# Optimization experiments

Measured on AMD Instinct MI355X. Metric: run time of the kernel, lower is better.

Reference implementation:

```python
import jax, jax.numpy as jnp
import numpy as np
from jax import lax


def _shifted(X, k, alpha):
    # alpha * roll(X, -k, 0) + (1 - alpha) * roll(X, -k-1, 0), via gather
    N = X.shape[0]
    idx = (jnp.arange(N) + k) % N
    return alpha * X[idx] + (1.0 - alpha) * X[(idx + 1) % N]


def _all_distances(D_q, D_p, steps):
    # steps: [S] float32 signed step values. Returns [S] mean L2 distances.
    N = D_q.shape[0]
    rows = jnp.arange(N)

    def dist_one(step):
        s = jnp.abs(step)
        k = jnp.floor(s).astype(jnp.int32)          # int(step) of |step|
        alpha = s - k.astype(step.dtype)
        diff = lax.cond(
            step >= 0,
            lambda: _shifted(D_q, k, alpha) - D_p,   # shift query forward
            lambda: D_q - _shifted(D_p, k, alpha),   # shift positive (ref) forward
        )
        norms = jnp.sqrt(jnp.sum(diff * diff, axis=-1))  # [N]
        valid = rows < (N - k)                       # rows [:N - int_step]
        return jnp.sum(jnp.where(valid, norms, 0.0)) / (N - k).astype(norms.dtype)

    def body(carry, step):
        return carry, dist_one(step)

    _, dists = lax.scan(body, None, steps)
    return dists


def setup_inputs() -> dict:
    key = jax.random.key(0)
    k1, k2 = jax.random.split(key)
    N, D = 100000, 256
    return {
        "D_q": jax.random.normal(k1, (N, D), dtype=jnp.float32),
        "D_p": jax.random.normal(k2, (N, D), dtype=jnp.float32),
        "max_step": 60,
        "step_size": 1,
    }


def reference(D_q, D_p, max_step, step_size):
    # Same candidate step schedule as the torch loop (static, built on host).
    steps_np = np.concatenate([
        np.arange(0, max_step, step_size),
        -np.arange(1, max_step + 1, step_size),
    ]).astype(np.float32)
    steps = jnp.asarray(steps_np)                    # [2*max_step/step_size]
    dists = _all_distances(D_q, D_p, steps)
    i = jnp.argmin(dists)
    return steps[i], dists[i]
```

## Files before the change

kernel.cpp:

```cpp
#include <hip/hip_runtime.h>
#include <math.h>


typedef __attribute__((ext_vector_type(8))) __bf16 bf16x8;
typedef __attribute__((ext_vector_type(16))) float f32x16;
typedef __attribute__((ext_vector_type(8))) unsigned short us8;

#define LDSH 280
#define PR 6
#define MAXS 128
#define NREP 32

#define LGKM_FENCE()                                                          \
  do {                                                                        \
    __builtin_amdgcn_sched_barrier(0);                                        \
    asm volatile("s_waitcnt lgkmcnt(0)" ::: "memory");                        \
    __builtin_amdgcn_sched_barrier(0);                                        \
  } while (0)

__device__ __forceinline__ unsigned short f2bf(float x) {
  return __builtin_bit_cast(unsigned short, (__bf16)x);
}

__device__ __forceinline__ int xcd_swz(int bid, int nwg) {
  const int q = nwg >> 3, r = nwg & 7;
  const int x = bid & 7, i = bid >> 3;
  return (x < r ? x * (q + 1) : r * (q + 1) + (x - r) * q) + i;
}

__global__ __launch_bounds__(576, 1)
void band_kernel(const float* __restrict__ Q, const float* __restrict__ P,
                 double* __restrict__ ws,
                 const int* __restrict__ msp, const int* __restrict__ ssp,
                 int N, int TS, int nsb, int gridB) {
  __shared__ __align__(16) unsigned short Bsh[PR * 32 * LDSH];
  __shared__ __align__(16) unsigned short Qsh[2 * 32 * LDSH];
  __shared__ float NpS[PR * 32];
  __shared__ float NqS[2 * 32];
  __shared__ float sums[MAXS];
  __shared__ float red[12];
  __shared__ int packs[2];

  const int t = threadIdx.x;
  const int lane = t & 63;
  const int wid = t >> 6;
  const int ms = msp[0], ss = ssp[0];
  const int S1 = (ms + ss - 1) / ss;
  const int S = 2 * S1;

  if (blockIdx.x >= gridB) {
    const int si = blockIdx.x - gridB;
    if (si >= S) return;
    int k, qr, pr;
    if (si < S1) { k = si * ss;            qr = 0;           pr = N - (k + 1); }
    else         { k = 1 + (si - S1) * ss; qr = N - (k + 1); pr = 0; }
    float sq = 0.f;
    if (t < 256) {
      const float e = Q[(size_t)qr * 256 + t] - P[(size_t)pr * 256 + t];
      sq = e * e;
    }
    #pragma unroll
    for (int off = 32; off >= 1; off >>= 1) sq += __shfl_xor(sq, off);
    if (lane == 0) red[wid] = sq;
    __syncthreads();
    if (t == 0) {
      float tot = 0.f;
      #pragma unroll
      for (int w = 0; w < 9; ++w) tot += red[w];
      ws[(size_t)NREP * MAXS + si] = (double)sqrtf(tot);
    }
    return;
  }

  const int sb = xcd_swz(blockIdx.x, gridB);
  const int T0 = sb * nsb;
  int ns = TS - T0; if (ns > nsb) ns = nsb;
  if (ns <= 0) return;

  for (int i = t; i < MAXS; i += 576) sums[i] = 0.f;
  if (t == 0) { packs[0] = 0; packs[1] = 0; }
  __syncthreads();

  volatile int* vprod = &packs[0];
  volatile int* vcons = &packs[1];

  if (wid >= 5) {
    const int pw = wid - 5;
    const int rr = pw * 8 + (lane >> 3);
    const int li = lane & 7;

    auto issueT = [&](const float* __restrict__ base, int tau, float4* v) {
      const int gr = tau * 32 + rr;
      if (gr >= 0 && gr < N) {
        const float* src = base + (size_t)gr * 256 + li * 8;
        #pragma unroll
        for (int j = 0; j < 4; ++j) {
          v[2 * j]     = *reinterpret_cast<const float4*>(src + j * 64);
          v[2 * j + 1] = *reinterpret_cast<const float4*>(src + j * 64 + 4);
        }
      } else {
        #pragma unroll
        for (int j = 0; j < 8; ++j) v[j] = make_float4(0.f, 0.f, 0.f, 0.f);
      }
    };

    auto commitT = [&](unsigned short* dst, float* ndst, int slot, const float4* v) {
      float nrm = 0.f;
      unsigned short* row = dst + slot * 32 * LDSH + rr * LDSH + li * 8;
      #pragma unroll
      for (int j = 0; j < 4; ++j) {
        const float f0 = v[2*j].x, f1 = v[2*j].y, f2 = v[2*j].z, f3 = v[2*j].w;
        const float f4 = v[2*j+1].x, f5 = v[2*j+1].y, f6 = v[2*j+1].z, f7 = v[2*j+1].w;
        nrm = fmaf(f0, f0, nrm); nrm = fmaf(f1, f1, nrm);
        nrm = fmaf(f2, f2, nrm); nrm = fmaf(f3, f3, nrm);
        nrm = fmaf(f4, f4, nrm); nrm = fmaf(f5, f5, nrm);
        nrm = fmaf(f6, f6, nrm); nrm = fmaf(f7, f7, nrm);
        us8 h;
        h[0] = f2bf(f0); h[1] = f2bf(f1); h[2] = f2bf(f2); h[3] = f2bf(f3);
        h[4] = f2bf(f4); h[5] = f2bf(f5); h[6] = f2bf(f6); h[7] = f2bf(f7);
        *reinterpret_cast<us8*>(row + j * 64) = h;
      }
      nrm += __shfl_xor(nrm, 1);
      nrm += __shfl_xor(nrm, 2);
      nrm += __shfl_xor(nrm, 4);
      if (li == 0) ndst[slot * 32 + rr] = nrm;
    };

    float4 Ap[8], Aq[8], Bp[8], Bq[8];
    const int JT = ns + 4;

#define P_ISSUE(JJ, SET)                                                      \
    { const int pj_ = (JJ);                                                   \
      if (pj_ < JT) {                                                         \
        issueT(P, T0 + pj_ - 2, SET##p);                                      \
        if (pj_ >= 4) issueT(Q, T0 + pj_ - 4, SET##q);                        \
      } }
#define P_STEP(JJ, SET)                                                       \
    { const int j_ = (JJ);                                                    \
      const int needc = j_ - 5;                                               \
      if (needc > 0) {                                                        \
        for (;;) {                                                            \
          const int v = *vcons;                                               \
          if ((v & 63) >= needc && ((v >> 6) & 63) >= needc &&                \
              ((v >> 12) & 63) >= needc && ((v >> 18) & 63) >= needc &&       \
              ((v >> 24) & 63) >= needc) break;                               \
          __builtin_amdgcn_s_sleep(1);                                        \
        }                                                                     \
      }                                                                       \
      commitT(Bsh, NpS, j_ % PR, SET##p);                                     \
      if (j_ >= 4) commitT(Qsh, NqS, (j_ - 4) & 1, SET##q);                   \
      LGKM_FENCE();                                                           \
      if (lane == 0) atomicAdd(&packs[0], 1 << (8 * pw));                     \
      P_ISSUE(j_ + 2, SET); }

    P_ISSUE(0, A);
    P_ISSUE(1, B);
    int j = 0;
    for (; j + 2 <= JT; j += 2) {
      P_STEP(j, A);
      P_STEP(j + 1, B);
    }
    if (j < JT) P_STEP(j, A);
#undef P_STEP
#undef P_ISSUE
  } else {
    const int l31 = lane & 31;
    const int hi = lane >> 5;

    int slotR[16];
    #pragma unroll
    for (int r = 0; r < 16; ++r) {
      const int arow = (r & 3) + 8 * (r >> 2) + 4 * hi;
      const int d = arow - l31 - (wid - 2) * 32;
      int slot = -1;
      if (d >= 1) {
        const int k = d - 1;
        if (k < ms && (k % ss) == 0) slot = k / ss;
      } else if (d <= -2) {
        const int kk = -d - 1;
        if (kk <= ms && ((kk - 1) % ss) == 0) slot = S1 + (kk - 1) / ss;
      }
      if (slot >= MAXS) slot = -1;
      slotR[r] = slot;
    }
    float racc[16];
    #pragma unroll
    for (int r = 0; r < 16; ++r) racc[r] = 0.f;

    #pragma unroll 1
    for (int s = 0; s < ns; ++s) {
      const int T = T0 + s;
      const int need = s + 5;
      for (;;) {
        const int v = *vprod;
        if ((v & 255) >= need && ((v >> 8) & 255) >= need &&
            ((v >> 16) & 255) >= need && ((v >> 24) & 255) >= need) break;
        __builtin_amdgcn_s_sleep(1);
      }
      __builtin_amdgcn_sched_barrier(0);

      const int tauW = T - 2 + wid;
      const int slotP = (s + wid) % PR;
      const int slotQ = s & 1;
      const unsigned short* Ab = &Qsh[slotQ * 32 * LDSH + l31 * LDSH + hi * 8];
      const unsigned short* Bb = &Bsh[slotP * 32 * LDSH + l31 * LDSH + hi * 8];
      f32x16 acc0 = {}, acc1 = {};
      __builtin_amdgcn_s_setprio(1);
      #pragma unroll
      for (int ks = 0; ks < 16; ks += 2) {
        const bf16x8 a0 = *reinterpret_cast<const bf16x8*>(Ab + ks * 16);
        const bf16x8 b0 = *reinterpret_cast<const bf16x8*>(Bb + ks * 16);
        const bf16x8 a1 = *reinterpret_cast<const bf16x8*>(Ab + ks * 16 + 16);
        const bf16x8 b1 = *reinterpret_cast<const bf16x8*>(Bb + ks * 16 + 16);
        acc0 = __builtin_amdgcn_mfma_f32_32x32x16_bf16(a0, b0, acc0, 0, 0, 0);
        acc1 = __builtin_amdgcn_mfma_f32_32x32x16_bf16(a1, b1, acc1, 0, 0, 0);
      }
      __builtin_amdgcn_s_setprio(0);

      const int bcol = tauW * 32 + l31;
      if (bcol >= 0 && bcol < N) {
        const float npW = NpS[slotP * 32 + l31];
        const int aT = T * 32;
        #pragma unroll
        for (int r = 0; r < 16; ++r) {
          const int arow = (r & 3) + 8 * (r >> 2) + 4 * hi;
          if (slotR[r] >= 0 && (aT + arow) < N) {
            const float n2 = NqS[slotQ * 32 + arow] + npW
                             - 2.0f * (acc0[r] + acc1[r]);
            racc[r] += sqrtf(fmaxf(n2, 0.f));
          }
        }
      }

      LGKM_FENCE();
      if (lane == 0) atomicAdd(&packs[1], 1 << (6 * wid));
    }

    #pragma unroll
    for (int r = 0; r < 16; ++r)
      if (slotR[r] >= 0 && racc[r] != 0.f) atomicAdd(&sums[slotR[r]], racc[r]);
  }

  __syncthreads();
  if (t < S && t < MAXS) {
    const float v = sums[t];
    if (v != 0.f)
      unsafeAtomicAdd(&ws[(size_t)(blockIdx.x & (NREP - 1)) * MAXS + t], (double)v);
  }
}

__global__ void finalize_kernel(const double* __restrict__ ws, float* __restrict__ out,
                                const int* __restrict__ msp, const int* __restrict__ ssp,
                                int N) {
  __shared__ double dist_sh[MAXS];
  const int t = threadIdx.x;
  const int ms = msp[0], ss = ssp[0];
  const int S1 = (ms + ss - 1) / ss;
  const int S = 2 * S1;
  if (t < S && t < MAXS) {
    double tot = 0.0;
    for (int rep = 0; rep < NREP; ++rep) tot += ws[(size_t)rep * MAXS + t];
    tot += ws[(size_t)NREP * MAXS + t];
    const int k = (t < S1) ? t * ss : 1 + (t - S1) * ss;
    dist_sh[t] = tot / (double)(N - k);
  }
  __syncthreads();
  if (t == 0) {
    int best = 0;
    double bd = dist_sh[0];
    for (int s = 1; s < S && s < MAXS; ++s)
      if (dist_sh[s] < bd) { bd = dist_sh[s]; best = s; }
    const int k = (best < S1) ? best * ss : 1 + (best - S1) * ss;
    out[0] = (best < S1) ? (float)k : -(float)k;
    out[1] = (float)bd;
  }
}

extern "C" void kernel_launch(void* const* d_in, const int* in_sizes, int n_in,
                              void* d_out, int out_size, void* d_ws, size_t ws_size,
                              hipStream_t stream) {
  const float* Q   = (const float*)d_in[0];
  const float* P   = (const float*)d_in[1];
  const int*   msp = (const int*)d_in[2];
  const int*   ssp = (const int*)d_in[3];
  const int N = in_sizes[0] / 256;
  double* ws = (double*)d_ws;

  hipMemsetAsync(d_ws, 0, (size_t)(NREP + 1) * MAXS * sizeof(double), stream);

  const int TS = (N + 31) / 32;
  int nsb = (TS + 249) / 250;
  if (nsb < 1) nsb = 1;
  if (nsb > 59) nsb = 59;
  const int gridB = (TS + nsb - 1) / nsb;

  band_kernel<<<gridB + MAXS, 576, 0, stream>>>(Q, P, ws, msp, ssp,
                                                N, TS, nsb, gridB);
  finalize_kernel<<<1, 128, 0, stream>>>(ws, (float*)d_out, msp, ssp, N);
}
```

Baseline: 64.54 us.

## Switch band MFMA from bf16 to fp8 e4m3 and rebalance block partition

Tiles staged in LDS are now stored as fp8 e4m3 bytes instead of bf16, and the dot products use the fp8 32x32x16 MFMA. This halves LDS footprint and LDS read traffic per tile. The grid also changes from a fixed 13-tile chunk per block to a fixed 512 blocks with a balanced start/end split, to spread work more evenly across CUs. The cost is much coarser precision in the dot-product term of the norm expansion, which could shift the argmin, and more blocks each paying the pipeline halo overhead.

```diff
diff --git a/kernel.cpp b/kernel.cpp
--- a/kernel.cpp
+++ b/kernel.cpp
@@ -1,12 +1,11 @@
 #include <hip/hip_runtime.h>
+#include <hip/hip_fp8.h>
 #include <math.h>
 
 
-typedef __attribute__((ext_vector_type(8))) __bf16 bf16x8;
 typedef __attribute__((ext_vector_type(16))) float f32x16;
-typedef __attribute__((ext_vector_type(8))) unsigned short us8;
-
-#define LDSH 280
+
+#define LDSB 272
 #define PR 6
 #define MAXS 128
 #define NREP 32
@@ -18,8 +17,9 @@
     __builtin_amdgcn_sched_barrier(0);                                        \
   } while (0)
 
-__device__ __forceinline__ unsigned short f2bf(float x) {
-  return __builtin_bit_cast(unsigned short, (__bf16)x);
+__device__ __forceinline__ unsigned char f2fp8(float x) {
+  __hip_fp8_e4m3 v(x);
+  return (unsigned char)v.__x;
 }
 
 __device__ __forceinline__ int xcd_swz(int bid, int nwg) {
@@ -32,9 +32,9 @@
 void band_kernel(const float* __restrict__ Q, const float* __restrict__ P,
                  double* __restrict__ ws,
                  const int* __restrict__ msp, const int* __restrict__ ssp,
-                 int N, int TS, int nsb, int gridB) {
-  __shared__ __align__(16) unsigned short Bsh[PR * 32 * LDSH];
-  __shared__ __align__(16) unsigned short Qsh[2 * 32 * LDSH];
+                 int N, int TS, int gridB) {
+  __shared__ __align__(16) unsigned char Bsh[PR * 32 * LDSB];
+  __shared__ __align__(16) unsigned char Qsh[2 * 32 * LDSB];
   __shared__ float NpS[PR * 32];
   __shared__ float NqS[2 * 32];
   __shared__ float sums[MAXS];
@@ -73,8 +73,9 @@
   }
 
   const int sb = xcd_swz(blockIdx.x, gridB);
-  const int T0 = sb * nsb;
-  int ns = TS - T0; if (ns > nsb) ns = nsb;
+  const int T0 = (int)(((long long)sb * TS) / gridB);
+  const int T1 = (int)(((long long)(sb + 1) * TS) / gridB);
+  const int ns = T1 - T0;
   if (ns <= 0) return;
 
   for (int i = t; i < MAXS; i += 576) sums[i] = 0.f;
@@ -104,9 +105,9 @@
       }
     };
 
-    auto commitT = [&](unsigned short* dst, float* ndst, int slot, const float4* v) {
+    auto commitT = [&](unsigned char* dst, float* ndst, int slot, const float4* v) {
       float nrm = 0.f;
-      unsigned short* row = dst + slot * 32 * LDSH + rr * LDSH + li * 8;
+      unsigned char* row = dst + slot * 32 * LDSB + rr * LDSB + li * 8;
       #pragma unroll
       for (int j = 0; j < 4; ++j) {
         const float f0 = v[2*j].x, f1 = v[2*j].y, f2 = v[2*j].z, f3 = v[2*j].w;
@@ -115,10 +116,16 @@
         nrm = fmaf(f2, f2, nrm); nrm = fmaf(f3, f3, nrm);
         nrm = fmaf(f4, f4, nrm); nrm = fmaf(f5, f5, nrm);
         nrm = fmaf(f6, f6, nrm); nrm = fmaf(f7, f7, nrm);
-        us8 h;
-        h[0] = f2bf(f0); h[1] = f2bf(f1); h[2] = f2bf(f2); h[3] = f2bf(f3);
-        h[4] = f2bf(f4); h[5] = f2bf(f5); h[6] = f2bf(f6); h[7] = f2bf(f7);
-        *reinterpret_cast<us8*>(row + j * 64) = h;
+        unsigned long long u =
+            (unsigned long long)f2fp8(f0)
+          | ((unsigned long long)f2fp8(f1) << 8)
+          | ((unsigned long long)f2fp8(f2) << 16)
+          | ((unsigned long long)f2fp8(f3) << 24)
+          | ((unsigned long long)f2fp8(f4) << 32)
+          | ((unsigned long long)f2fp8(f5) << 40)
+          | ((unsigned long long)f2fp8(f6) << 48)
+          | ((unsigned long long)f2fp8(f7) << 56);
+        *reinterpret_cast<unsigned long long*>(row + j * 64) = u;
       }
       nrm += __shfl_xor(nrm, 1);
       nrm += __shfl_xor(nrm, 2);
@@ -202,18 +209,18 @@
       const int tauW = T - 2 + wid;
       const int slotP = (s + wid) % PR;
       const int slotQ = s & 1;
-      const unsigned short* Ab = &Qsh[slotQ * 32 * LDSH + l31 * LDSH + hi * 8];
-      const unsigned short* Bb = &Bsh[slotP * 32 * LDSH + l31 * LDSH + hi * 8];
+      const unsigned char* Ab = &Qsh[slotQ * 32 * LDSB + l31 * LDSB + hi * 8];
+      const unsigned char* Bb = &Bsh[slotP * 32 * LDSB + l31 * LDSB + hi * 8];
       f32x16 acc0 = {}, acc1 = {};
       __builtin_amdgcn_s_setprio(1);
       #pragma unroll
       for (int ks = 0; ks < 16; ks += 2) {
-        const bf16x8 a0 = *reinterpret_cast<const bf16x8*>(Ab + ks * 16);
-        const bf16x8 b0 = *reinterpret_cast<const bf16x8*>(Bb + ks * 16);
-        const bf16x8 a1 = *reinterpret_cast<const bf16x8*>(Ab + ks * 16 + 16);
-        const bf16x8 b1 = *reinterpret_cast<const bf16x8*>(Bb + ks * 16 + 16);
-        acc0 = __builtin_amdgcn_mfma_f32_32x32x16_bf16(a0, b0, acc0, 0, 0, 0);
-        acc1 = __builtin_amdgcn_mfma_f32_32x32x16_bf16(a1, b1, acc1, 0, 0, 0);
+        const long long a0 = *reinterpret_cast<const long long*>(Ab + ks * 16);
+        const long long b0 = *reinterpret_cast<const long long*>(Bb + ks * 16);
+        const long long a1 = *reinterpret_cast<const long long*>(Ab + ks * 16 + 16);
+        const long long b1 = *reinterpret_cast<const long long*>(Bb + ks * 16 + 16);
+        acc0 = __builtin_amdgcn_mfma_f32_32x32x16_fp8_fp8(a0, b0, acc0, 0, 0, 0);
+        acc1 = __builtin_amdgcn_mfma_f32_32x32x16_fp8_fp8(a1, b1, acc1, 0, 0, 0);
       }
       __builtin_amdgcn_s_setprio(0);
 
@@ -289,12 +296,10 @@
   hipMemsetAsync(d_ws, 0, (size_t)(NREP + 1) * MAXS * sizeof(double), stream);
 
   const int TS = (N + 31) / 32;
-  int nsb = (TS + 249) / 250;
-  if (nsb < 1) nsb = 1;
-  if (nsb > 59) nsb = 59;
-  const int gridB = (TS + nsb - 1) / nsb;
+  int gridB = 512;
+  if (gridB > TS) gridB = TS;
 
   band_kernel<<<gridB + MAXS, 576, 0, stream>>>(Q, P, ws, msp, ssp,
-                                                N, TS, nsb, gridB);
+                                                N, TS, gridB);
   finalize_kernel<<<1, 128, 0, stream>>>(ws, (float*)d_out, msp, ssp, N);
 }
```

Result: slower. 86.89 us (+34.6%).
